# Optimization experiments

Hardware: AMD Instinct MI355X
Metric: run time of the kernel (lower is better)

The kernel has to match this reference:

```python
import jax, jax.numpy as jnp
import numpy as np

HIDDEN = 4096
NUM_HEADS = 32
HEAD_DIM = HIDDEN // NUM_HEADS  # 128
ROPE_THETA = 10000.0
MAX_POS = 2048


def _rope_tables():
    inv_freq = 1.0 / (ROPE_THETA ** (jnp.arange(0, HEAD_DIM, 2, dtype=jnp.float32) / HEAD_DIM))
    t = jnp.arange(MAX_POS, dtype=jnp.float32)
    freqs = jnp.einsum('i,j->ij', t, inv_freq)          # [MAX_POS, HEAD_DIM/2]
    emb = jnp.concatenate([freqs, freqs], axis=-1)      # [MAX_POS, HEAD_DIM]
    return jnp.cos(emb), jnp.sin(emb)


def _apply_rotary(x, cos, sin):
    # x: [b, s, h, d]; cos/sin: [b, s, 1, d]
    half = x.shape[-1] // 2
    x_rot = jnp.concatenate([-x[..., half:], x[..., :half]], axis=-1)
    return x * cos + x_rot * sin


def setup_inputs() -> dict:
    key = jax.random.key(0)
    k1, k2, k3, k4, k5 = jax.random.split(key, 5)
    B, S = 1, 2048
    scale = 1.0 / np.sqrt(HIDDEN)
    return {
        'hidden_states': jax.random.normal(k1, (B, S, HIDDEN), dtype=jnp.float32),
        'position_ids': jnp.arange(S, dtype=jnp.int64).reshape(1, S),
        'wqkv_w': jax.random.normal(k2, (3 * HIDDEN, HIDDEN), dtype=jnp.float32) * scale,
        'wqkv_b': jax.random.normal(k3, (3 * HIDDEN,), dtype=jnp.float32) * 0.01,
        'wo_w': jax.random.normal(k4, (HIDDEN, HIDDEN), dtype=jnp.float32) * scale,
        'wo_b': jax.random.normal(k5, (HIDDEN,), dtype=jnp.float32) * 0.01,
    }


def reference(hidden_states, position_ids, wqkv_w, wqkv_b, wo_w, wo_b):
    b, s, _ = hidden_states.shape
    qkv = hidden_states @ wqkv_w.T + wqkv_b                  # [b, s, 3*hidden]
    qkv = qkv.reshape(b, s, NUM_HEADS, 3, HEAD_DIM)          # (h g d) layout
    q, k, v = qkv[..., 0, :], qkv[..., 1, :], qkv[..., 2, :]  # [b, s, h, d]

    cos_tab, sin_tab = _rope_tables()
    cos = cos_tab[position_ids][:, :, None, :]               # [b_or_1, s, 1, d]
    sin = sin_tab[position_ids][:, :, None, :]
    q = _apply_rotary(q, cos, sin)
    k = _apply_rotary(k, cos, sin)

    scores = jnp.einsum('bqhd,bkhd->bhqk', q, k) / jnp.sqrt(jnp.float32(HEAD_DIM))
    causal = jnp.tril(jnp.ones((s, s), dtype=bool))
    scores = jnp.where(causal[None, None, :, :], scores, -jnp.inf)
    attn = jax.nn.softmax(scores, axis=-1)
    out = jnp.einsum('bhqk,bkhd->bqhd', attn, v).reshape(b, s, HIDDEN)
    return out @ wo_w.T + wo_b
```

## Files before the change

kernel.cpp:

```cpp
#include <hip/hip_runtime.h>
#include <hip/hip_bf16.h>

typedef short bf16x8 __attribute__((ext_vector_type(8)));
typedef float f32x4  __attribute__((ext_vector_type(4)));

typedef __attribute__((address_space(1))) const unsigned int gu32_t;
typedef __attribute__((address_space(3))) unsigned int lu32_t;

__device__ inline void gld16(const void* g, void* l) {
  __builtin_amdgcn_global_load_lds((gu32_t*)g, (lu32_t*)l, 16, 0, 0);
}

#define S_LEN 2048
#define HID   4096
#define NH    32
#define HD    128
#define QKV_N 12288

__global__ void cvt_bf16_kernel(const float* __restrict__ in,
                                __hip_bfloat16* __restrict__ out, long n) {
  long stride = (long)gridDim.x * blockDim.x;
  for (long i = (long)blockIdx.x * blockDim.x + threadIdx.x; i * 8 < n; i += stride) {
    long b = i * 8;
    float4 a0 = *(const float4*)(in + b);
    float4 a1 = *(const float4*)(in + b + 4);
    union { __hip_bfloat16 h[8]; bf16x8 v; } u;
    u.h[0] = __float2bfloat16(a0.x); u.h[1] = __float2bfloat16(a0.y);
    u.h[2] = __float2bfloat16(a0.z); u.h[3] = __float2bfloat16(a0.w);
    u.h[4] = __float2bfloat16(a1.x); u.h[5] = __float2bfloat16(a1.y);
    u.h[6] = __float2bfloat16(a1.z); u.h[7] = __float2bfloat16(a1.w);
    *(bf16x8*)(out + b) = u.v;
  }
}

template<int WRITE_BF16>
__global__ __launch_bounds__(256) void gemm_bt_kernel(
    const __hip_bfloat16* __restrict__ A,
    const __hip_bfloat16* __restrict__ B,
    const float* __restrict__ bias,
    void* __restrict__ Cout, int M, int N, int K)
{
  __shared__ __hip_bfloat16 lA[128 * 64];
  __shared__ __hip_bfloat16 lB[128 * 64];
  const int t = threadIdx.x;
  const int w = t >> 6, l = t & 63;
  const int lr = l & 15, lg = l >> 4;
  const int m0 = blockIdx.x * 128, n0 = blockIdx.y * 128;
  const int wm = (w >> 1) * 64, wn = (w & 1) * 64;

  f32x4 acc[4][4] = {};

  for (int k0 = 0; k0 < K; k0 += 64) {
    #pragma unroll
    for (int i = 0; i < 4; ++i) {
      int c = i * 256 + t;
      int row = c >> 3, s = c & 7;
      gld16(A + (long)(m0 + row) * K + k0 + (s ^ (row & 7)) * 8, &lA[c * 8]);
    }
    #pragma unroll
    for (int i = 0; i < 4; ++i) {
      int c = i * 256 + t;
      int row = c >> 3, s = c & 7;
      gld16(B + (long)(n0 + row) * K + k0 + (s ^ (row & 7)) * 8, &lB[c * 8]);
    }
    __syncthreads();
    #pragma unroll
    for (int ks = 0; ks < 2; ++ks) {
      bf16x8 af[4], bfr[4];
      #pragma unroll
      for (int mi = 0; mi < 4; ++mi) {
        int row = wm + mi * 16 + lr;
        af[mi] = *(const bf16x8*)&lA[row * 64 + ((ks * 4 + lg) ^ (row & 7)) * 8];
      }
      #pragma unroll
      for (int ni = 0; ni < 4; ++ni) {
        int row = wn + ni * 16 + lr;
        bfr[ni] = *(const bf16x8*)&lB[row * 64 + ((ks * 4 + lg) ^ (row & 7)) * 8];
      }
      #pragma unroll
      for (int mi = 0; mi < 4; ++mi)
        #pragma unroll
        for (int ni = 0; ni < 4; ++ni)
          acc[mi][ni] = __builtin_amdgcn_mfma_f32_16x16x32_bf16(af[mi], bfr[ni], acc[mi][ni], 0, 0, 0);
    }
    __syncthreads();
  }

  #pragma unroll
  for (int mi = 0; mi < 4; ++mi) {
    #pragma unroll
    for (int ni = 0; ni < 4; ++ni) {
      int col = n0 + wn + ni * 16 + lr;
      float bv = bias[col];
      #pragma unroll
      for (int r = 0; r < 4; ++r) {
        int row = m0 + wm + mi * 16 + lg * 4 + r;
        float v = acc[mi][ni][r] + bv;
        if (WRITE_BF16)
          ((__hip_bfloat16*)Cout)[(long)row * N + col] = __float2bfloat16(v);
        else
          ((float*)Cout)[(long)row * N + col] = v;
      }
    }
  }
}

__global__ void rope_table_kernel(const int* __restrict__ pos,
                                  float* __restrict__ ct, float* __restrict__ st) {
  int s = blockIdx.x, j = threadIdx.x;
  float p = (float)pos[s];
  float invf = exp2f(-0.20762050593046013f * (float)j);
  float a = p * invf;
  ct[s * 64 + j] = cosf(a);
  st[s * 64 + j] = sinf(a);
}

__global__ __launch_bounds__(256) void rope_rearrange_kernel(
    const __hip_bfloat16* __restrict__ qkv,
    const float* __restrict__ ct, const float* __restrict__ st,
    __hip_bfloat16* __restrict__ Qr, __hip_bfloat16* __restrict__ Kr,
    __hip_bfloat16* __restrict__ Vt)
{
  __shared__ __hip_bfloat16 lv[64][136];
  const int h = blockIdx.y, s0 = blockIdx.x * 64, t = threadIdx.x;
  #pragma unroll
  for (int i = 0; i < 16; ++i) {
    int idx = i * 256 + t;
    int si = idx >> 6, j = idx & 63;
    long base = (long)(s0 + si) * QKV_N + h * 384;
    float c  = ct[(s0 + si) * 64 + j];
    float sn = st[(s0 + si) * 64 + j];
    float q1 = __bfloat162float(qkv[base + j]);
    float q2 = __bfloat162float(qkv[base + 64 + j]);
    float k1 = __bfloat162float(qkv[base + 128 + j]);
    float k2 = __bfloat162float(qkv[base + 192 + j]);
    long ob = (long)h * (S_LEN * HD) + (long)(s0 + si) * HD;
    Qr[ob + j]      = __float2bfloat16(q1 * c - q2 * sn);
    Qr[ob + 64 + j] = __float2bfloat16(q2 * c + q1 * sn);
    Kr[ob + j]      = __float2bfloat16(k1 * c - k2 * sn);
    Kr[ob + 64 + j] = __float2bfloat16(k2 * c + k1 * sn);
    lv[si][j]      = qkv[base + 256 + j];
    lv[si][64 + j] = qkv[base + 320 + j];
  }
  __syncthreads();
  #pragma unroll
  for (int i = 0; i < 4; ++i) {
    int c = i * 256 + t;
    int d = c >> 3, s8 = (c & 7) * 8;
    union { __hip_bfloat16 h8[8]; bf16x8 v; } u;
    #pragma unroll
    for (int j2 = 0; j2 < 8; ++j2) u.h8[j2] = lv[s8 + j2][d];
    *(bf16x8*)(Vt + (long)h * (HD * S_LEN) + (long)d * S_LEN + s0 + s8) = u.v;
  }
}

#define FA_STAGE(buf, k0_) do {                                              \
    _Pragma("unroll")                                                        \
    for (int i_ = 0; i_ < 4; ++i_) {               \
      int c_ = i_ * 256 + t;                                                 \
      int row_ = c_ >> 4, s_ = c_ & 15;                                      \
      gld16(Kh + (long)((k0_) + row_) * HD + (s_ ^ (row_ & 15)) * 8,         \
            &lK[buf][c_ * 8]);                                               \
    }                                                                        \
    _Pragma("unroll")                                                        \
    for (int i_ = 0; i_ < 4; ++i_) {             \
      int c_ = i_ * 256 + t;                                                 \
      int d_ = c_ >> 3, s_ = c_ & 7;                                         \
      gld16(Vh + (long)d_ * S_LEN + (k0_) + (s_ ^ (d_ & 7)) * 8,             \
            &lV[buf][c_ * 8]);                                               \
    } } while (0)

__global__ __launch_bounds__(256) void flash_attn_kernel(
    const __hip_bfloat16* __restrict__ Qr, const __hip_bfloat16* __restrict__ Kr,
    const __hip_bfloat16* __restrict__ Vt, __hip_bfloat16* __restrict__ O)
{
  __shared__ __hip_bfloat16 lK[2][64 * 128];
  __shared__ __hip_bfloat16 lV[2][128 * 64];
  __shared__ __hip_bfloat16 lP[4][16 * 72];
  const int h = blockIdx.y, pair = blockIdx.x;
  const int t = threadIdx.x, w = t >> 6, l = t & 63;
  const int lr = l & 15, lg = l >> 4;
  const __hip_bfloat16* Qh = Qr + (long)h * (S_LEN * HD);
  const __hip_bfloat16* Kh = Kr + (long)h * (S_LEN * HD);
  const __hip_bfloat16* Vh = Vt + (long)h * (HD * S_LEN);
  const float sc = 0.08838834764831845f;

  for (int ph = 0; ph < 2; ++ph) {
    const int qt = ph ? (31 - pair) : pair;
    const int q0 = qt * 64;

    bf16x8 qf[4];
    #pragma unroll
    for (int ks = 0; ks < 4; ++ks)
      qf[ks] = *(const bf16x8*)(Qh + (long)(q0 + w * 16 + lr) * HD + ks * 32 + lg * 8);

    float m_r[4], l_r[4];
    f32x4 oacc[8] = {};
    #pragma unroll
    for (int r = 0; r < 4; ++r) { m_r[r] = -1e30f; l_r[r] = 0.f; }

    const int ktiles = qt + 1;
    int cur = 0;
    FA_STAGE(0, 0);
    __syncthreads();

    for (int kt = 0; kt < ktiles; ++kt) {
      const int k0 = kt * 64;
      if (kt + 1 < ktiles) FA_STAGE(cur ^ 1, k0 + 64);

      f32x4 s[4] = {};
      #pragma unroll
      for (int ks = 0; ks < 4; ++ks) {
        bf16x8 kf[4];
        #pragma unroll
        for (int nf = 0; nf < 4; ++nf) {
          int row = nf * 16 + lr;
          kf[nf] = *(const bf16x8*)&lK[cur][row * 128 + ((ks * 4 + lg) ^ (row & 15)) * 8];
        }
        #pragma unroll
        for (int nf = 0; nf < 4; ++nf)
          s[nf] = __builtin_amdgcn_mfma_f32_16x16x32_bf16(qf[ks], kf[nf], s[nf], 0, 0, 0);
      }

      #pragma unroll
      for (int r = 0; r < 4; ++r) {
        int q = q0 + w * 16 + lg * 4 + r;
        float mx = -1e30f;
        #pragma unroll
        for (int nf = 0; nf < 4; ++nf) {
          int k = k0 + nf * 16 + lr;
          float v = s[nf][r] * sc;
          if (k > q) v = -1e30f;
          s[nf][r] = v;
          mx = fmaxf(mx, v);
        }
        #pragma unroll
        for (int mk = 1; mk < 16; mk <<= 1) mx = fmaxf(mx, __shfl_xor(mx, mk));
        float mo = m_r[r];
        float mn = fmaxf(mo, mx);
        m_r[r] = mn;
        float alpha = __expf(mo - mn);
        float rs = 0.f;
        #pragma unroll
        for (int nf = 0; nf < 4; ++nf) {
          float p = __expf(s[nf][r] - mn);
          s[nf][r] = p;
          rs += p;
        }
        #pragma unroll
        for (int mk = 1; mk < 16; mk <<= 1) rs += __shfl_xor(rs, mk);
        l_r[r] = l_r[r] * alpha + rs;
        #pragma unroll
        for (int df = 0; df < 8; ++df) oacc[df][r] *= alpha;
      }

      #pragma unroll
      for (int nf = 0; nf < 4; ++nf)
        #pragma unroll
        for (int r = 0; r < 4; ++r)
          lP[w][(lg * 4 + r) * 72 + nf * 16 + lr] = __float2bfloat16(s[nf][r]);
      asm volatile("s_waitcnt lgkmcnt(0)" ::: "memory");

      #pragma unroll
      for (int ks2 = 0; ks2 < 2; ++ks2) {
        bf16x8 pa = *(const bf16x8*)&lP[w][lr * 72 + ks2 * 32 + lg * 8];
        #pragma unroll
        for (int df = 0; df < 8; ++df) {
          int row = df * 16 + lr;
          bf16x8 vf = *(const bf16x8*)&lV[cur][row * 64 + ((ks2 * 4 + lg) ^ (row & 7)) * 8];
          oacc[df] = __builtin_amdgcn_mfma_f32_16x16x32_bf16(pa, vf, oacc[df], 0, 0, 0);
        }
      }
      __syncthreads();
      cur ^= 1;
    }

    #pragma unroll
    for (int r = 0; r < 4; ++r) {
      float inv = 1.f / l_r[r];
      long q = q0 + w * 16 + lg * 4 + r;
      #pragma unroll
      for (int df = 0; df < 8; ++df)
        O[q * HID + h * HD + df * 16 + lr] = __float2bfloat16(oacc[df][r] * inv);
    }
    __syncthreads();
  }
}

extern "C" void kernel_launch(void* const* d_in, const int* in_sizes, int n_in,
                              void* d_out, int out_size, void* d_ws, size_t ws_size,
                              hipStream_t stream)
{
  (void)in_sizes; (void)n_in; (void)out_size;
  const float* hidden = (const float*)d_in[0];
  const int*   pos    = (const int*)d_in[1];
  const float* wqkv_w = (const float*)d_in[2];
  const float* wqkv_b = (const float*)d_in[3];
  const float* wo_w   = (const float*)d_in[4];
  const float* wo_b   = (const float*)d_in[5];
  float* out = (float*)d_out;

  char* ws = (char*)d_ws;
  if (ws_size < 167772160UL) return;
  __hip_bfloat16* hid_bf  = (__hip_bfloat16*)(ws + 0);
  __hip_bfloat16* wqkv_bf = (__hip_bfloat16*)(ws + 16777216);
  __hip_bfloat16* qr      = (__hip_bfloat16*)(ws + 0);
  __hip_bfloat16* kr      = (__hip_bfloat16*)(ws + 16777216);
  __hip_bfloat16* vt      = (__hip_bfloat16*)(ws + 33554432);
  __hip_bfloat16* obf     = (__hip_bfloat16*)(ws + 50331648);
  __hip_bfloat16* wo_bf   = (__hip_bfloat16*)(ws + 67108864);
  float*          cos_t   = (float*)(ws + 100663296);
  float*          sin_t   = (float*)(ws + 100663296 + 524288);
  __hip_bfloat16* qkv_bf  = (__hip_bfloat16*)(ws + 117440512);

  cvt_bf16_kernel<<<4096, 256, 0, stream>>>(hidden, hid_bf, 8388608L);
  cvt_bf16_kernel<<<8192, 256, 0, stream>>>(wqkv_w, wqkv_bf, 50331648L);
  gemm_bt_kernel<1><<<dim3(16, 96), 256, 0, stream>>>(hid_bf, wqkv_bf, wqkv_b, qkv_bf, 2048, 12288, 4096);
  cvt_bf16_kernel<<<8192, 256, 0, stream>>>(wo_w, wo_bf, 16777216L);
  rope_table_kernel<<<2048, 64, 0, stream>>>(pos, cos_t, sin_t);
  rope_rearrange_kernel<<<dim3(32, 32), 256, 0, stream>>>(qkv_bf, cos_t, sin_t, qr, kr, vt);
  flash_attn_kernel<<<dim3(16, 32), 256, 0, stream>>>(qr, kr, vt, obf);
  gemm_bt_kernel<0><<<dim3(16, 32), 256, 0, stream>>>(obf, wo_bf, wo_b, out, 2048, 4096, 4096);
}
```

Before: 489.1 us.

## Use exp2 softmax, mask only diagonal tile, and lazily rescale running max

Folds log2(e) into the score scale so exponentials use exp2f. Causal masking now runs only on the diagonal key tile instead of every tile. The running-max update, with its cross-lane reductions and the rescale of the accumulator, is skipped unless some row's tile max exceeds the stored max by more than 8 (in log2 units). This removes shuffles and multiplies from most iterations, but lets unnormalized exponentials grow up to 2^8, which relies on fp32 range and bf16 P precision.

```diff
diff --git a/kernel.cpp b/kernel.cpp
--- a/kernel.cpp
+++ b/kernel.cpp
@@ -183,7 +183,7 @@
   const __hip_bfloat16* Qh = Qr + (long)h * (S_LEN * HD);
   const __hip_bfloat16* Kh = Kr + (long)h * (S_LEN * HD);
   const __hip_bfloat16* Vh = Vt + (long)h * (HD * S_LEN);
-  const float sc = 0.08838834764831845f;
+  const float sc2 = 0.12751744f;
 
   for (int ph = 0; ph < 2; ++ph) {
     const int qt = ph ? (31 - pair) : pair;
@@ -222,36 +222,60 @@
           s[nf] = __builtin_amdgcn_mfma_f32_16x16x32_bf16(qf[ks], kf[nf], s[nf], 0, 0, 0);
       }
 
-      #pragma unroll
-      for (int r = 0; r < 4; ++r) {
-        int q = q0 + w * 16 + lg * 4 + r;
-        float mx = -1e30f;
+      if (kt == qt) {
         #pragma unroll
         for (int nf = 0; nf < 4; ++nf) {
           int k = k0 + nf * 16 + lr;
-          float v = s[nf][r] * sc;
-          if (k > q) v = -1e30f;
-          s[nf][r] = v;
-          mx = fmaxf(mx, v);
-        }
-        #pragma unroll
-        for (int mk = 1; mk < 16; mk <<= 1) mx = fmaxf(mx, __shfl_xor(mx, mk));
-        float mo = m_r[r];
-        float mn = fmaxf(mo, mx);
-        m_r[r] = mn;
-        float alpha = __expf(mo - mn);
+          #pragma unroll
+          for (int r = 0; r < 4; ++r) {
+            int q = q0 + w * 16 + lg * 4 + r;
+            float v = s[nf][r] * sc2;
+            s[nf][r] = (k > q) ? -1e30f : v;
+          }
+        }
+      } else {
+        #pragma unroll
+        for (int nf = 0; nf < 4; ++nf)
+          #pragma unroll
+          for (int r = 0; r < 4; ++r)
+            s[nf][r] *= sc2;
+      }
+
+      bool need = false;
+      float lm[4];
+      #pragma unroll
+      for (int r = 0; r < 4; ++r) {
+        lm[r] = fmaxf(fmaxf(s[0][r], s[1][r]), fmaxf(s[2][r], s[3][r]));
+        need = need || (lm[r] > m_r[r] + 8.f);
+      }
+      if (__any((int)need)) {
+        #pragma unroll
+        for (int r = 0; r < 4; ++r) {
+          float mx = lm[r];
+          #pragma unroll
+          for (int mk = 1; mk < 16; mk <<= 1) mx = fmaxf(mx, __shfl_xor(mx, mk));
+          float mo = m_r[r];
+          float mn = fmaxf(mo, mx);
+          float alpha = exp2f(mo - mn);
+          m_r[r] = mn;
+          l_r[r] *= alpha;
+          #pragma unroll
+          for (int df = 0; df < 8; ++df) oacc[df][r] *= alpha;
+        }
+      }
+
+      #pragma unroll
+      for (int r = 0; r < 4; ++r) {
         float rs = 0.f;
         #pragma unroll
         for (int nf = 0; nf < 4; ++nf) {
-          float p = __expf(s[nf][r] - mn);
+          float p = exp2f(s[nf][r] - m_r[r]);
           s[nf][r] = p;
           rs += p;
         }
         #pragma unroll
         for (int mk = 1; mk < 16; mk <<= 1) rs += __shfl_xor(rs, mk);
-        l_r[r] = l_r[r] * alpha + rs;
-        #pragma unroll
-        for (int df = 0; df < 8; ++df) oacc[df][r] *= alpha;
+        l_r[r] += rs;
       }
 
       #pragma unroll
```

Result: no change. 484.8 us (-0.9%).
